# Performance work log

Measured on AMD Instinct MI355X. Metric: run time of the kernel, lower is better.

The kernel has to match this reference:

```python
import jax, jax.numpy as jnp
import numpy as np

N, P, E = 100000, 10000, 500000
DN, DP, DK, SKIP, MLP_H = 256, 128, 100, 27, 64
E_MEAN, E_STD = 4.0, 2.0
ETA_MEAN, ETA_STD = 0.0, 1.5
ATT_NORM = 0.1  # 1/sqrt(100)
LN_EPS, RMS_EPS = 1e-5, 1e-6


def setup_inputs() -> dict:
    key = jax.random.key(0)
    ks = jax.random.split(key, 32)
    DIN = DN + SKIP  # 283
    s = 0.05
    inp = {
        'node_hidden': jax.random.normal(ks[0], (N, DN), jnp.float32),
        'energy': jax.random.uniform(ks[1], (N,), jnp.float32, 0.01, 1.0),
        'eta': jax.random.normal(ks[2], (N,), jnp.float32),
        'phi': jax.random.normal(ks[3], (N,), jnp.float32),
        'layer': jax.random.uniform(ks[4], (N,), jnp.float32),
        'eta_l': jax.random.normal(ks[5], (N, 6), jnp.float32),
        'phi_l': jax.random.normal(ks[6], (N, 6), jnp.float32),
        'ene_l': jax.random.normal(ks[7], (N, 6), jnp.float32),
        'track_feats': jax.random.uniform(ks[8], (N, 5), jnp.float32),
        'particle_hidden': jax.random.normal(ks[9], (P, DP), jnp.float32),
        'global_rep': jax.random.normal(ks[10], (P, DN), jnp.float32),
        'edge_src': jax.random.randint(ks[11], (E,), 0, N, jnp.int32),
        'edge_dst': jax.random.randint(ks[12], (E,), 0, P, jnp.int32),
        # learned params
        'W_key': jax.random.normal(ks[13], (DIN, DK), jnp.float32) * s,
        'b_key': jnp.zeros((DK,), jnp.float32),
        'W_val': jax.random.normal(ks[14], (DIN, DP), jnp.float32) * s,
        'b_val': jnp.zeros((DP,), jnp.float32),
        'W_q': jax.random.normal(ks[15], (DP + DN, DK), jnp.float32) * s,
        'b_q': jnp.zeros((DK,), jnp.float32),
        'W_ih': jax.random.normal(ks[16], (DP, 3 * DP), jnp.float32) * s,
        'b_ih': jnp.zeros((3 * DP,), jnp.float32),
        'W_hh': jax.random.normal(ks[17], (DP, 3 * DP), jnp.float32) * s,
        'b_hh': jnp.zeros((3 * DP,), jnp.float32),
        'ln_g': jnp.ones((DP,), jnp.float32),
        'ln_b': jnp.zeros((DP,), jnp.float32),
        'W1': jax.random.normal(ks[18], (DP, MLP_H), jnp.float32) * s,
        'b1': jnp.zeros((MLP_H,), jnp.float32),
        'W2': jax.random.normal(ks[19], (MLP_H, DP), jnp.float32) * s,
        'b2': jnp.zeros((DP,), jnp.float32),
        'rms_w': jnp.ones((DP,), jnp.float32),
        'lin_w': jax.random.normal(ks[20], (1, DP), jnp.float32),
    }
    return inp


def _forward(node_hidden, energy, eta, phi, layer, eta_l, phi_l, ene_l, track_feats,
             particle_hidden, global_rep,
             W_key, b_key, W_val, b_val, W_q, b_q, W_ih, b_ih, W_hh, b_hh,
             ln_g, ln_b, W1, b1, W2, b2, rms_w, lin_w, edge_src, edge_dst):
    # --- build node inputs: hidden rep + 27 skip scalars (same order as torch cat) ---
    skip = jnp.concatenate([
        ((jnp.log(energy) - E_MEAN) / E_STD)[:, None],
        ((eta - ETA_MEAN) / ETA_STD)[:, None],
        phi[:, None], layer[:, None],
        (eta_l - ETA_MEAN) / ETA_STD,  # eta_l1..l6
        phi_l, ene_l,
        track_feats,  # isTrack, nTracks, tracks_pt, nTracks_4, tracks_pt_4
    ], axis=1)  # [N, 27]
    x = jnp.concatenate([node_hidden, skip], axis=1)  # [N, 283]
    keys = x @ W_key + b_key      # [N, 100]
    vals = x @ W_val + b_val      # [N, DP]
    q = jnp.concatenate([particle_hidden, global_rep], axis=1) @ W_q + b_q  # [P, 100]

    # --- per-edge attention (note: node_update consumes RAW relu attention) ---
    att = jax.nn.relu(jnp.sum(keys[edge_src] * q[edge_dst], axis=1) * ATT_NORM)  # [E]
    msg = att[:, None] * vals[edge_src]                                          # [E, DP]
    ws = jax.ops.segment_sum(msg, edge_dst, num_segments=P)                      # [P, DP]

    # --- node update: rmsnorm * sigmoid(eltwise) gating, GRU, LN, MLP residual ---
    rms = ws * jax.lax.rsqrt(jnp.mean(ws * ws, axis=-1, keepdims=True) + RMS_EPS) * rms_w
    gated = rms * jax.nn.sigmoid(ws * lin_w)

    h = particle_hidden
    gi = gated @ W_ih + b_ih
    gh = h @ W_hh + b_hh
    i_r, i_z, i_n = jnp.split(gi, 3, axis=1)
    h_r, h_z, h_n = jnp.split(gh, 3, axis=1)
    r = jax.nn.sigmoid(i_r + h_r)
    z = jax.nn.sigmoid(i_z + h_z)
    n = jnp.tanh(i_n + r * h_n)
    h_new = (1.0 - z) * n + z * h

    mu = jnp.mean(h_new, axis=-1, keepdims=True)
    var = jnp.mean((h_new - mu) ** 2, axis=-1, keepdims=True)
    ln = (h_new - mu) * jax.lax.rsqrt(var + LN_EPS) * ln_g + ln_b
    mlp = jax.nn.relu(ln @ W1 + b1) @ W2 + b2
    return h + mlp  # updated particle 'node hidden rep'


def reference(node_hidden, energy, eta, phi, layer, eta_l, phi_l, ene_l, track_feats,
              particle_hidden, global_rep, edge_src, edge_dst,
              W_key, b_key, W_val, b_val, W_q, b_q, W_ih, b_ih, W_hh, b_hh,
              ln_g, ln_b, W1, b1, W2, b2, rms_w, lin_w):
    return _forward(node_hidden, energy, eta, phi, layer, eta_l, phi_l, ene_l, track_feats,
                    particle_hidden, global_rep,
                    W_key, b_key, W_val, b_val, W_q, b_q, W_ih, b_ih, W_hh, b_hh,
                    ln_g, ln_b, W1, b1, W2, b2, rms_w, lin_w, edge_src, edge_dst)
```

## Files before the change

### kernel.cpp

```cpp
#include <hip/hip_runtime.h>
#include <hip/hip_bf16.h>
#include <math.h>

#define THREADS 256

typedef __bf16 bf16_t;
typedef __bf16 bf16x8 __attribute__((ext_vector_type(8)));
typedef float f32x4 __attribute__((ext_vector_type(4)));

__device__ __forceinline__ float sigmoidf_(float x) { return 1.f / (1.f + expf(-x)); }

__device__ __forceinline__ void gload_lds16(const void* g, void* l) {
    __builtin_amdgcn_global_load_lds((const __attribute__((address_space(1))) void*)g,
                                     (__attribute__((address_space(3))) void*)l, 16, 0, 0);
}

__device__ __forceinline__ bf16x8 cvt8(float4 a, float4 b) {
    bf16x8 v;
    v[0] = (bf16_t)a.x; v[1] = (bf16_t)a.y; v[2] = (bf16_t)a.z; v[3] = (bf16_t)a.w;
    v[4] = (bf16_t)b.x; v[5] = (bf16_t)b.y; v[6] = (bf16_t)b.z; v[7] = (bf16_t)b.w;
    return v;
}

__global__ void prep_kernel(const float* __restrict__ W_key, const float* __restrict__ W_val,
                            const float* __restrict__ W_q, const float* __restrict__ b_key,
                            const float* __restrict__ b_val, const float* __restrict__ b_q,
                            bf16_t* __restrict__ WbfT, bf16_t* __restrict__ WqT,
                            float* __restrict__ bpn, float* __restrict__ bpq)
{
    int i = blockIdx.x * THREADS + threadIdx.x;
    const int NW = 256 * 288, NQ = 128 * 384;
    if (i < NW) {
        int c = i / 288, k = i - c * 288;
        float v = 0.f;
        if (k < 283) {
            if (c < 100) v = W_key[k * 100 + c];
            else if (c >= 128 && c < 256) v = W_val[k * 128 + (c - 128)];
        }
        WbfT[i] = (bf16_t)v;
    } else if (i < NW + NQ) {
        int j = i - NW;
        int c = j / 384, k = j - c * 384;
        WqT[j] = (bf16_t)((c < 100) ? W_q[k * 100 + c] : 0.f);
    } else if (i < NW + NQ + 256) {
        int c = i - NW - NQ;
        bpn[c] = (c < 100) ? b_key[c] : ((c >= 128 && c < 256) ? b_val[c - 128] : 0.f);
    } else if (i < NW + NQ + 256 + 128) {
        int c = i - NW - NQ - 256;
        bpq[c] = (c < 100) ? b_q[c] : 0.f;
    }
}

__global__ void prep2_kernel(const float* __restrict__ W_ih, const float* __restrict__ W_hh,
                             const float* __restrict__ b_ih, const float* __restrict__ b_hh,
                             const float* __restrict__ W1, const float* __restrict__ b1,
                             const float* __restrict__ W2,
                             bf16_t* __restrict__ BTg, bf16_t* __restrict__ W1Tp,
                             bf16_t* __restrict__ W2Tp, float* __restrict__ bgru,
                             float* __restrict__ b1p,
                             int* __restrict__ cnt, int twoP,
                             bf16_t* __restrict__ AG, int padStart, int padElems)
{
    int i = blockIdx.x * THREADS + threadIdx.x;
    const int NG = 768 * 256, N1 = 128 * 128, N2 = 128 * 128;
    const int NB = NG + N1 + N2 + 768 + 128;
    if (i < NG) {
        int c = i >> 8, k = i & 255;
        float v = 0.f;
        if (c < 384) { if (k < 128) v = W_ih[k * 384 + c]; }
        else         { if (k >= 128) v = W_hh[(k - 128) * 384 + (c - 384)]; }
        BTg[i] = (bf16_t)v;
    } else if (i < NG + N1) {
        int j = i - NG; int c = j >> 7, k = j & 127;
        W1Tp[j] = (bf16_t)((c < 64) ? W1[k * 64 + c] : 0.f);
    } else if (i < NG + N1 + N2) {
        int j = i - NG - N1; int c = j >> 7, k = j & 127;
        W2Tp[j] = (bf16_t)((k < 64) ? W2[k * 128 + c] : 0.f);
    } else if (i < NG + N1 + N2 + 768) {
        int c = i - NG - N1 - N2;
        bgru[c] = (c < 384) ? b_ih[c] : b_hh[c - 384];
    } else if (i < NB) {
        int c = i - NG - N1 - N2 - 768;
        b1p[c] = (c < 64) ? b1[c] : 0.f;
    } else if (i < NB + twoP) {
        cnt[i - NB] = 0;
    } else if (i < NB + twoP + padElems) {
        int j = i - NB - twoP;
        AG[(size_t)padStart * 256 + j] = (bf16_t)0.f;
    }
}

__global__ void skip_kernel(const float* __restrict__ energy, const float* __restrict__ eta,
                            const float* __restrict__ phi, const float* __restrict__ layer,
                            const float* __restrict__ eta_l, const float* __restrict__ phi_l,
                            const float* __restrict__ ene_l, const float* __restrict__ track,
                            bf16_t* __restrict__ skipb, int N_, int Mpad)
{
    int n = blockIdx.x * THREADS + threadIdx.x;
    if (n >= Mpad) return;
    float o[32];
#pragma unroll
    for (int j = 0; j < 32; ++j) o[j] = 0.f;
    if (n < N_) {
        o[0] = (logf(energy[n]) - 4.0f) * 0.5f;
        o[1] = eta[n] * (1.f / 1.5f);
        o[2] = phi[n];
        o[3] = layer[n];
#pragma unroll
        for (int j = 0; j < 6; ++j) o[4 + j]  = eta_l[n * 6 + j] * (1.f / 1.5f);
#pragma unroll
        for (int j = 0; j < 6; ++j) o[10 + j] = phi_l[n * 6 + j];
#pragma unroll
        for (int j = 0; j < 6; ++j) o[16 + j] = ene_l[n * 6 + j];
#pragma unroll
        for (int j = 0; j < 5; ++j) o[22 + j] = track[n * 5 + j];
    }
    bf16_t* dst = skipb + (size_t)n * 32;
#pragma unroll
    for (int g = 0; g < 4; ++g) {
        bf16x8 v;
#pragma unroll
        for (int j = 0; j < 8; ++j) v[j] = (bf16_t)o[g * 8 + j];
        *(bf16x8*)(dst + g * 8) = v;
    }
}

template <int MODE>
__global__ __launch_bounds__(256) void mfma_gemm(
    const void* __restrict__ A0, const void* __restrict__ A1,
    const bf16_t* __restrict__ BT, const float* __restrict__ bias,
    void* __restrict__ out0v, const float* __restrict__ resid,
    int K, int Mlimit, int Nrows)
{
    __shared__ short AsS[64 * 32];
    __shared__ short BsS[128 * 32];
    int tid = threadIdx.x;
    int lane = tid & 63, w = tid >> 6;
    int la = lane & 15, hi = lane >> 4;
    int m0 = (w & 1) * 32, n0 = (w >> 1) * 64;
    int row0 = blockIdx.y * 64, col0 = blockIdx.x * 128;

    f32x4 zero4 = {0.f, 0.f, 0.f, 0.f};
    f32x4 acc[2][4];
#pragma unroll
    for (int i = 0; i < 2; ++i)
#pragma unroll
        for (int j = 0; j < 4; ++j) acc[i][j] = zero4;

    const int ra = tid >> 2, ka = (tid & 3) * 8;
    const int c1 = tid + 256;
    const int rb0 = tid >> 2, kb0 = (tid & 3) * 8;
    const int rb1 = c1 >> 2,  kb1 = (c1 & 3) * 8;

    for (int kt = 0; kt < K; kt += 32) {
        int gmA = row0 + ra;
        if (MODE == 0) {
            if (kt < 256) {
                bf16x8 v = {};
                if (gmA < Nrows) {
                    const float* s = (const float*)A0 + (size_t)gmA * 256 + kt + ka;
                    v = cvt8(*(const float4*)s, *(const float4*)(s + 4));
                }
                *(bf16x8*)(AsS + (size_t)tid * 8) = v;
            } else {
                gload_lds16((const bf16_t*)A1 + (size_t)gmA * 32 + (kt - 256) + ka,
                            AsS + (size_t)tid * 8);
            }
        } else if (MODE == 1) {
            int gk = kt + ka;
            bf16x8 v = {};
            if (gmA < Nrows) {
                const float* s = (gk < 128) ? ((const float*)A0 + (size_t)gmA * 128 + gk)
                                            : ((const float*)A1 + (size_t)gmA * 256 + (gk - 128));
                v = cvt8(*(const float4*)s, *(const float4*)(s + 4));
            }
            *(bf16x8*)(AsS + (size_t)tid * 8) = v;
        } else {
            gload_lds16((const bf16_t*)A0 + (size_t)gmA * K + kt + ka,
                        AsS + (size_t)tid * 8);
        }
        gload_lds16(BT + (size_t)(col0 + rb0) * K + kt + kb0, BsS + (size_t)tid * 8);
        gload_lds16(BT + (size_t)(col0 + rb1) * K + kt + kb1, BsS + (size_t)c1 * 8);
        __syncthreads();
        bf16x8 a[2], b[4];
#pragma unroll
        for (int i = 0; i < 2; ++i)
            a[i] = *(const bf16x8*)(AsS + (m0 + i * 16 + la) * 32 + hi * 8);
#pragma unroll
        for (int j = 0; j < 4; ++j)
            b[j] = *(const bf16x8*)(BsS + (n0 + j * 16 + la) * 32 + hi * 8);
#pragma unroll
        for (int i = 0; i < 2; ++i)
#pragma unroll
            for (int j = 0; j < 4; ++j)
                acc[i][j] = __builtin_amdgcn_mfma_f32_16x16x32_bf16(a[i], b[j], acc[i][j], 0, 0, 0);
        __syncthreads();
    }

#pragma unroll
    for (int i = 0; i < 2; ++i) {
#pragma unroll
        for (int j = 0; j < 4; ++j) {
            int col = col0 + n0 + j * 16 + la;
            float bb = bias[col];
#pragma unroll
            for (int r = 0; r < 4; ++r) {
                int row = row0 + m0 + i * 16 + hi * 4 + r;
                float v = acc[i][j][r] + bb;
                if (MODE == 0) {
                    ((bf16_t*)out0v)[(size_t)row * 256 + col] = (bf16_t)v;
                } else if (MODE == 1) {
                    ((bf16_t*)out0v)[(size_t)row * 128 + col] = (bf16_t)v;
                } else if (MODE == 2) {
                    ((float*)out0v)[(size_t)row * 768 + col] = v;
                } else if (MODE == 3) {
                    ((bf16_t*)out0v)[(size_t)row * 128 + col] = (bf16_t)fmaxf(v, 0.f);
                } else {
                    if (row < Mlimit)
                        ((float*)out0v)[(size_t)row * 128 + col] = v + resid[(size_t)row * 128 + col];
                }
            }
        }
    }
}

__global__ void hist_kernel(const int* __restrict__ dst, int* __restrict__ cnt, int E_)
{
    int i = blockIdx.x * THREADS + threadIdx.x;
    if (i < E_) atomicAdd(&cnt[dst[i]], 1);
}

__global__ void scan_kernel(const int* __restrict__ cnt, int* __restrict__ offb, int P_)
{
    __shared__ int wsum[16];
    int tid = threadIdx.x;
    int lane = tid & 63, w = tid >> 6;
    int base = tid * 10;
    int c[10];
    int s = 0;
#pragma unroll
    for (int j = 0; j < 10; ++j) {
        int i = base + j;
        c[j] = (i < P_) ? cnt[i] : 0;
        s += c[j];
    }
    int pre = s;
    for (int o = 1; o < 64; o <<= 1) {
        int t = __shfl_up(pre, o);
        if (lane >= o) pre += t;
    }
    if (lane == 63) wsum[w] = pre;
    __syncthreads();
    if (w == 0 && lane < 16) {
        int v = wsum[lane];
        for (int o = 1; o < 16; o <<= 1) {
            int t = __shfl_up(v, o, 16);
            if (lane >= o) v += t;
        }
        wsum[lane] = v;
    }
    __syncthreads();
    int waveoff = (w == 0) ? 0 : wsum[w - 1];
    int run = waveoff + pre - s;
#pragma unroll
    for (int j = 0; j < 10; ++j) {
        int i = base + j;
        if (i <= P_) offb[i] = run;
        run += c[j];
    }
}

__global__ void fill_src_kernel(const int* __restrict__ dst, const int* __restrict__ src,
                                const int* __restrict__ offb, int* __restrict__ cur,
                                int* __restrict__ csrc, int E_)
{
    int i = blockIdx.x * THREADS + threadIdx.x;
    if (i < E_) {
        int d = dst[i];
        int pos = atomicAdd(&cur[d], 1);
        csrc[offb[d] + pos] = src[i];
    }
}

__global__ __launch_bounds__(256) void edge_kernel(
    const int* __restrict__ offb, const int* __restrict__ csrc,
    const bf16_t* __restrict__ KVb, const bf16_t* __restrict__ Qb,
    const float* __restrict__ ph, const float* __restrict__ rms_w,
    const float* __restrict__ lin_w, bf16_t* __restrict__ AG, int P_)
{
    int tid = threadIdx.x;
    int p = blockIdx.x * 4 + (tid >> 6);
    if (p >= P_) return;
    int lane = tid & 63;
    int c = lane & 15, g = lane >> 4;

    bf16x8 q8 = *(const bf16x8*)(Qb + (size_t)p * 128 + c * 8);
    float qf[8];
#pragma unroll
    for (int j = 0; j < 8; ++j) qf[j] = (float)q8[j];

    int s0 = offb[p], e0 = offb[p + 1];
    float acc[8] = {};

    int i = s0 + g;
    for (; i + 12 < e0; i += 16) {
        int n0 = csrc[i], n1 = csrc[i + 4], n2 = csrc[i + 8], n3 = csrc[i + 12];
        const bf16_t* b0 = KVb + (size_t)n0 * 256 + c * 8;
        const bf16_t* b1 = KVb + (size_t)n1 * 256 + c * 8;
        const bf16_t* b2 = KVb + (size_t)n2 * 256 + c * 8;
        const bf16_t* b3 = KVb + (size_t)n3 * 256 + c * 8;
        bf16x8 k0 = *(const bf16x8*)b0, v0 = *(const bf16x8*)(b0 + 128);
        bf16x8 k1 = *(const bf16x8*)b1, v1 = *(const bf16x8*)(b1 + 128);
        bf16x8 k2 = *(const bf16x8*)b2, v2 = *(const bf16x8*)(b2 + 128);
        bf16x8 k3 = *(const bf16x8*)b3, v3 = *(const bf16x8*)(b3 + 128);
        float d0 = 0.f, d1 = 0.f, d2 = 0.f, d3 = 0.f;
#pragma unroll
        for (int j = 0; j < 8; ++j) {
            d0 += qf[j] * (float)k0[j]; d1 += qf[j] * (float)k1[j];
            d2 += qf[j] * (float)k2[j]; d3 += qf[j] * (float)k3[j];
        }
        d0 += __shfl_xor(d0, 1); d1 += __shfl_xor(d1, 1); d2 += __shfl_xor(d2, 1); d3 += __shfl_xor(d3, 1);
        d0 += __shfl_xor(d0, 2); d1 += __shfl_xor(d1, 2); d2 += __shfl_xor(d2, 2); d3 += __shfl_xor(d3, 2);
        d0 += __shfl_xor(d0, 4); d1 += __shfl_xor(d1, 4); d2 += __shfl_xor(d2, 4); d3 += __shfl_xor(d3, 4);
        d0 += __shfl_xor(d0, 8); d1 += __shfl_xor(d1, 8); d2 += __shfl_xor(d2, 8); d3 += __shfl_xor(d3, 8);
        float a0 = fmaxf(d0 * 0.1f, 0.f), a1 = fmaxf(d1 * 0.1f, 0.f);
        float a2 = fmaxf(d2 * 0.1f, 0.f), a3 = fmaxf(d3 * 0.1f, 0.f);
#pragma unroll
        for (int j = 0; j < 8; ++j)
            acc[j] += a0 * (float)v0[j] + a1 * (float)v1[j]
                    + a2 * (float)v2[j] + a3 * (float)v3[j];
    }
    for (; i < e0; i += 4) {
        int nA = csrc[i];
        const bf16_t* bA = KVb + (size_t)nA * 256 + c * 8;
        bf16x8 kA = *(const bf16x8*)bA;
        bf16x8 vA = *(const bf16x8*)(bA + 128);
        float dA = 0.f;
#pragma unroll
        for (int j = 0; j < 8; ++j) dA += qf[j] * (float)kA[j];
        dA += __shfl_xor(dA, 1);
        dA += __shfl_xor(dA, 2);
        dA += __shfl_xor(dA, 4);
        dA += __shfl_xor(dA, 8);
        float aA = fmaxf(dA * 0.1f, 0.f);
#pragma unroll
        for (int j = 0; j < 8; ++j) acc[j] += aA * (float)vA[j];
    }

#pragma unroll
    for (int j = 0; j < 8; ++j) {
        acc[j] += __shfl_xor(acc[j], 16);
        acc[j] += __shfl_xor(acc[j], 32);
    }

    float ss = 0.f;
#pragma unroll
    for (int j = 0; j < 8; ++j) ss += acc[j] * acc[j];
    ss += __shfl_xor(ss, 1); ss += __shfl_xor(ss, 2); ss += __shfl_xor(ss, 4); ss += __shfl_xor(ss, 8);
    float scale = rsqrtf(ss * (1.f / 128.f) + 1e-6f);
    if (g == 0) {
        int cb = c * 8;
        const float* hp = ph + (size_t)p * 128 + cb;
        float4 ha = *(const float4*)hp, hb = *(const float4*)(hp + 4);
        float hv[8] = {ha.x, ha.y, ha.z, ha.w, hb.x, hb.y, hb.z, hb.w};
        bf16x8 gv, hvb;
#pragma unroll
        for (int j = 0; j < 8; ++j) {
            float wsv = acc[j];
            float rv = wsv * scale * rms_w[cb + j];
            gv[j] = (bf16_t)(rv * sigmoidf_(wsv * lin_w[cb + j]));
            hvb[j] = (bf16_t)hv[j];
        }
        *(bf16x8*)(AG + (size_t)p * 256 + cb) = gv;
        *(bf16x8*)(AG + (size_t)p * 256 + 128 + cb) = hvb;
    }
}

__global__ void gru_ln_kernel(const float* __restrict__ G768, const float* __restrict__ ph,
                              const float* __restrict__ ln_g, const float* __restrict__ ln_b,
                              bf16_t* __restrict__ LNb, int P_, int Mq)
{
    int tid = threadIdx.x;
    int g = tid >> 4, s = tid & 15;
    int p = blockIdx.x * 16 + g;
    if (p >= Mq) return;
    int cb = s * 8;
    if (p >= P_) {
        bf16x8 z = {};
        *(bf16x8*)(LNb + (size_t)p * 128 + cb) = z;
        return;
    }
    const float* G = G768 + (size_t)p * 768;
    float ir[8], iz[8], in_[8], hr[8], hz[8], hn_[8], hv[8];
#pragma unroll
    for (int q = 0; q < 2; ++q) {
        float4 v;
        v = *(const float4*)(G + cb + q * 4);        ir[q*4]=v.x; ir[q*4+1]=v.y; ir[q*4+2]=v.z; ir[q*4+3]=v.w;
        v = *(const float4*)(G + 128 + cb + q * 4);  iz[q*4]=v.x; iz[q*4+1]=v.y; iz[q*4+2]=v.z; iz[q*4+3]=v.w;
        v = *(const float4*)(G + 256 + cb + q * 4);  in_[q*4]=v.x; in_[q*4+1]=v.y; in_[q*4+2]=v.z; in_[q*4+3]=v.w;
        v = *(const float4*)(G + 384 + cb + q * 4);  hr[q*4]=v.x; hr[q*4+1]=v.y; hr[q*4+2]=v.z; hr[q*4+3]=v.w;
        v = *(const float4*)(G + 512 + cb + q * 4);  hz[q*4]=v.x; hz[q*4+1]=v.y; hz[q*4+2]=v.z; hz[q*4+3]=v.w;
        v = *(const float4*)(G + 640 + cb + q * 4);  hn_[q*4]=v.x; hn_[q*4+1]=v.y; hn_[q*4+2]=v.z; hn_[q*4+3]=v.w;
        v = *(const float4*)(ph + (size_t)p * 128 + cb + q * 4);
        hv[q*4]=v.x; hv[q*4+1]=v.y; hv[q*4+2]=v.z; hv[q*4+3]=v.w;
    }
    float hn[8];
    float sm = 0.f, sq = 0.f;
#pragma unroll
    for (int j = 0; j < 8; ++j) {
        float r = sigmoidf_(ir[j] + hr[j]);
        float z = sigmoidf_(iz[j] + hz[j]);
        float n = tanhf(in_[j] + r * hn_[j]);
        hn[j] = (1.f - z) * n + z * hv[j];
        sm += hn[j]; sq += hn[j] * hn[j];
    }
    sm += __shfl_xor(sm, 1); sm += __shfl_xor(sm, 2); sm += __shfl_xor(sm, 4); sm += __shfl_xor(sm, 8);
    sq += __shfl_xor(sq, 1); sq += __shfl_xor(sq, 2); sq += __shfl_xor(sq, 4); sq += __shfl_xor(sq, 8);
    float mu = sm * (1.f / 128.f);
    float var = sq * (1.f / 128.f) - mu * mu;
    float iv = rsqrtf(var + 1e-5f);
    bf16x8 o;
#pragma unroll
    for (int j = 0; j < 8; ++j) {
        int c = cb + j;
        o[j] = (bf16_t)((hn[j] - mu) * iv * ln_g[c] + ln_b[c]);
    }
    *(bf16x8*)(LNb + (size_t)p * 128 + cb) = o;
}

extern "C" void kernel_launch(void* const* d_in, const int* in_sizes, int n_in,
                              void* d_out, int out_size, void* d_ws, size_t ws_size,
                              hipStream_t stream)
{
    const float* nh      = (const float*)d_in[0];
    const float* energy  = (const float*)d_in[1];
    const float* eta     = (const float*)d_in[2];
    const float* phi     = (const float*)d_in[3];
    const float* layer   = (const float*)d_in[4];
    const float* eta_l   = (const float*)d_in[5];
    const float* phi_l   = (const float*)d_in[6];
    const float* ene_l   = (const float*)d_in[7];
    const float* track   = (const float*)d_in[8];
    const float* ph      = (const float*)d_in[9];
    const float* grep    = (const float*)d_in[10];
    const int*   esrc    = (const int*)d_in[11];
    const int*   edst    = (const int*)d_in[12];
    const float* W_key   = (const float*)d_in[13];
    const float* b_key   = (const float*)d_in[14];
    const float* W_val   = (const float*)d_in[15];
    const float* b_val   = (const float*)d_in[16];
    const float* W_q     = (const float*)d_in[17];
    const float* b_q     = (const float*)d_in[18];
    const float* W_ih    = (const float*)d_in[19];
    const float* b_ih    = (const float*)d_in[20];
    const float* W_hh    = (const float*)d_in[21];
    const float* b_hh    = (const float*)d_in[22];
    const float* ln_g    = (const float*)d_in[23];
    const float* ln_b    = (const float*)d_in[24];
    const float* W1      = (const float*)d_in[25];
    const float* b1      = (const float*)d_in[26];
    const float* W2      = (const float*)d_in[27];
    const float* b2      = (const float*)d_in[28];
    const float* rms_w   = (const float*)d_in[29];
    const float* lin_w   = (const float*)d_in[30];

    const int N = in_sizes[1];
    const int P = in_sizes[9] / 128;
    const int E = in_sizes[11];
    const int Mpad = ((N + 127) / 128) * 128;
    const int Mq   = ((P + 127) / 128) * 128;

    char* base = (char*)d_ws;
    size_t off = 0;
    auto alloc = [&](size_t bytes) { void* p = base + off; off = (off + bytes + 255) & ~(size_t)255; return p; };
    bf16_t* skipb = (bf16_t*)alloc((size_t)Mpad * 32 * 2);
    bf16_t* WbfT  = (bf16_t*)alloc(256 * 288 * 2);
    bf16_t* WqT   = (bf16_t*)alloc(128 * 384 * 2);
    float*  bpn   = (float*)alloc(256 * 4);
    float*  bpq   = (float*)alloc(128 * 4);
    bf16_t* KVb   = (bf16_t*)alloc((size_t)Mpad * 256 * 2);
    bf16_t* Qb    = (bf16_t*)alloc((size_t)Mq * 128 * 2);
    int*    cnt   = (int*)alloc((size_t)(2 * P) * 4);
    int*    cur   = cnt + P;
    int*    offb  = (int*)alloc((size_t)(P + 1) * 4);
    int*    csrc  = (int*)alloc((size_t)E * 4);
    bf16_t* AG    = (bf16_t*)alloc((size_t)Mq * 256 * 2);
    bf16_t* BTg   = (bf16_t*)alloc(768 * 256 * 2);
    bf16_t* W1Tp  = (bf16_t*)alloc(128 * 128 * 2);
    bf16_t* W2Tp  = (bf16_t*)alloc(128 * 128 * 2);
    float*  bgru  = (float*)alloc(768 * 4);
    float*  b1p   = (float*)alloc(128 * 4);
    float*  G768  = (float*)alloc((size_t)Mq * 768 * 4);
    bf16_t* LNb   = (bf16_t*)alloc((size_t)Mq * 128 * 2);
    bf16_t* M1    = (bf16_t*)alloc((size_t)Mq * 128 * 2);

    {
        int total = 256 * 288 + 128 * 384 + 256 + 128;
        prep_kernel<<<(total + THREADS - 1) / THREADS, THREADS, 0, stream>>>(
            W_key, W_val, W_q, b_key, b_val, b_q, WbfT, WqT, bpn, bpq);
        int padElems = (Mq - P) * 256;
        int total2 = 768 * 256 + 128 * 128 + 128 * 128 + 768 + 128 + 2 * P + padElems;
        prep2_kernel<<<(total2 + THREADS - 1) / THREADS, THREADS, 0, stream>>>(
            W_ih, W_hh, b_ih, b_hh, W1, b1, W2, BTg, W1Tp, W2Tp, bgru, b1p,
            cnt, 2 * P, AG, P, padElems);
        skip_kernel<<<(Mpad + THREADS - 1) / THREADS, THREADS, 0, stream>>>(
            energy, eta, phi, layer, eta_l, phi_l, ene_l, track, skipb, N, Mpad);
    }
    mfma_gemm<0><<<dim3(2, Mpad / 64), THREADS, 0, stream>>>(
        nh, skipb, WbfT, bpn, KVb, nullptr, 288, 0, N);
    mfma_gemm<1><<<dim3(1, Mq / 64), THREADS, 0, stream>>>(
        ph, grep, WqT, bpq, Qb, nullptr, 384, 0, P);
    hist_kernel<<<(E + THREADS - 1) / THREADS, THREADS, 0, stream>>>(edst, cnt, E);
    scan_kernel<<<1, 1024, 0, stream>>>(cnt, offb, P);
    fill_src_kernel<<<(E + THREADS - 1) / THREADS, THREADS, 0, stream>>>(
        edst, esrc, offb, cur, csrc, E);
    edge_kernel<<<(P + 3) / 4, THREADS, 0, stream>>>(
        offb, csrc, KVb, Qb, ph, rms_w, lin_w, AG, P);
    mfma_gemm<2><<<dim3(6, Mq / 64), THREADS, 0, stream>>>(
        AG, nullptr, BTg, bgru, G768, nullptr, 256, 0, Mq);
    gru_ln_kernel<<<Mq / 16, THREADS, 0, stream>>>(G768, ph, ln_g, ln_b, LNb, P, Mq);
    mfma_gemm<3><<<dim3(1, Mq / 64), THREADS, 0, stream>>>(
        LNb, nullptr, W1Tp, b1p, M1, nullptr, 128, 0, Mq);
    mfma_gemm<4><<<dim3(1, Mq / 64), THREADS, 0, stream>>>(
        M1, nullptr, W2Tp, b2, d_out, ph, 128, P, Mq);
}
```

Measured before the change: 231.1 us.

## Replace KV GEMM with register-direct kernel covering all 256 output columns

Adds a dedicated kv_gemm kernel in which each block computes a 32-row by 256-column tile, so every node_hidden row is read and converted to bf16 only once instead of twice across two column blocks. A and B fragments are loaded straight from global memory into registers in MFMA layout, which removes the LDS staging and both __syncthreads per K step. In exchange, B weight reads are uncoalesced strided loads that rely on the cache, and there is no overlap of loads with MFMA work.

Result: slower. 263.9 us (+14.2%).

```diff
diff --git a/kernel.cpp b/kernel.cpp
--- a/kernel.cpp
+++ b/kernel.cpp
@@ -125,6 +125,64 @@
     }
 }
 
+__global__ __launch_bounds__(256) void kv_gemm(
+    const float* __restrict__ nh, const bf16_t* __restrict__ skipb,
+    const bf16_t* __restrict__ BT, const float* __restrict__ bias,
+    bf16_t* __restrict__ KVb, int N_)
+{
+    int tid = threadIdx.x;
+    int w = tid >> 6, lane = tid & 63;
+    int la = lane & 15, hi = lane >> 4;
+    int row0 = blockIdx.x * 32;
+    int col0 = w * 64;
+    int r0 = row0 + la, r1 = row0 + 16 + la;
+    bool ok0 = r0 < N_, ok1 = r1 < N_;
+    const float* pa0 = nh + (size_t)r0 * 256 + hi * 8;
+    const float* pa1 = nh + (size_t)r1 * 256 + hi * 8;
+
+    f32x4 zero4 = {0.f, 0.f, 0.f, 0.f};
+    f32x4 acc[2][4];
+#pragma unroll
+    for (int i = 0; i < 2; ++i)
+#pragma unroll
+        for (int j = 0; j < 4; ++j) acc[i][j] = zero4;
+
+    for (int kt = 0; kt < 288; kt += 32) {
+        bf16x8 a0, a1;
+        if (kt < 256) {
+            bf16x8 z = {};
+            a0 = ok0 ? cvt8(*(const float4*)(pa0 + kt), *(const float4*)(pa0 + kt + 4)) : z;
+            a1 = ok1 ? cvt8(*(const float4*)(pa1 + kt), *(const float4*)(pa1 + kt + 4)) : z;
+        } else {
+            a0 = *(const bf16x8*)(skipb + (size_t)r0 * 32 + hi * 8);
+            a1 = *(const bf16x8*)(skipb + (size_t)r1 * 32 + hi * 8);
+        }
+        bf16x8 b[4];
+#pragma unroll
+        for (int j = 0; j < 4; ++j)
+            b[j] = *(const bf16x8*)(BT + (size_t)(col0 + j * 16 + la) * 288 + kt + hi * 8);
+#pragma unroll
+        for (int j = 0; j < 4; ++j) {
+            acc[0][j] = __builtin_amdgcn_mfma_f32_16x16x32_bf16(a0, b[j], acc[0][j], 0, 0, 0);
+            acc[1][j] = __builtin_amdgcn_mfma_f32_16x16x32_bf16(a1, b[j], acc[1][j], 0, 0, 0);
+        }
+    }
+
+#pragma unroll
+    for (int j = 0; j < 4; ++j) {
+        int col = col0 + j * 16 + la;
+        float bb = bias[col];
+#pragma unroll
+        for (int i = 0; i < 2; ++i) {
+#pragma unroll
+            for (int r = 0; r < 4; ++r) {
+                int row = row0 + i * 16 + hi * 4 + r;
+                KVb[(size_t)row * 256 + col] = (bf16_t)(acc[i][j][r] + bb);
+            }
+        }
+    }
+}
+
 template <int MODE>
 __global__ __launch_bounds__(256) void mfma_gemm(
     const void* __restrict__ A0, const void* __restrict__ A1,
@@ -154,19 +212,7 @@
 
     for (int kt = 0; kt < K; kt += 32) {
         int gmA = row0 + ra;
-        if (MODE == 0) {
-            if (kt < 256) {
-                bf16x8 v = {};
-                if (gmA < Nrows) {
-                    const float* s = (const float*)A0 + (size_t)gmA * 256 + kt + ka;
-                    v = cvt8(*(const float4*)s, *(const float4*)(s + 4));
-                }
-                *(bf16x8*)(AsS + (size_t)tid * 8) = v;
-            } else {
-                gload_lds16((const bf16_t*)A1 + (size_t)gmA * 32 + (kt - 256) + ka,
-                            AsS + (size_t)tid * 8);
-            }
-        } else if (MODE == 1) {
+        if (MODE == 1) {
             int gk = kt + ka;
             bf16x8 v = {};
             if (gmA < Nrows) {
@@ -207,9 +253,7 @@
             for (int r = 0; r < 4; ++r) {
                 int row = row0 + m0 + i * 16 + hi * 4 + r;
                 float v = acc[i][j][r] + bb;
-                if (MODE == 0) {
-                    ((bf16_t*)out0v)[(size_t)row * 256 + col] = (bf16_t)v;
-                } else if (MODE == 1) {
+                if (MODE == 1) {
                     ((bf16_t*)out0v)[(size_t)row * 128 + col] = (bf16_t)v;
                 } else if (MODE == 2) {
                     ((float*)out0v)[(size_t)row * 768 + col] = v;
@@ -506,8 +550,7 @@
         skip_kernel<<<(Mpad + THREADS - 1) / THREADS, THREADS, 0, stream>>>(
             energy, eta, phi, layer, eta_l, phi_l, ene_l, track, skipb, N, Mpad);
     }
-    mfma_gemm<0><<<dim3(2, Mpad / 64), THREADS, 0, stream>>>(
-        nh, skipb, WbfT, bpn, KVb, nullptr, 288, 0, N);
+    kv_gemm<<<Mpad / 32, THREADS, 0, stream>>>(nh, skipb, WbfT, bpn, KVb, N);
     mfma_gemm<1><<<dim3(1, Mq / 64), THREADS, 0, stream>>>(
         ph, grep, WqT, bpq, Qb, nullptr, 384, 0, P);
     hist_kernel<<<(E + THREADS - 1) / THREADS, THREADS, 0, stream>>>(edst, cnt, E);
```
